# Kernel optimization log

Measured on AMD Instinct MI355X. Metric: run time of the kernel, lower is better.

The kernel has to match this reference:

```python
import jax, jax.numpy as jnp
import numpy as np


def setup_inputs() -> dict:
    key = jax.random.key(0)
    k1, k2, k3, k4 = jax.random.split(key, 4)
    B, S, D = 4, 2048, 1024
    return {
        "x": jax.random.normal(k1, (B, S, D), dtype=jnp.float32),
        "wq": jax.random.normal(k2, (D, D), dtype=jnp.float32),
        "wk": jax.random.normal(k3, (D, D), dtype=jnp.float32),
        "wv": jax.random.normal(k4, (D, D), dtype=jnp.float32),
    }


def reference(x, wq, wk, wv):
    # q,k,v: [B,S,D]
    q = x @ wq
    k = x @ wk
    v = x @ wv
    # NOTE: source applies NO 1/sqrt(d) scaling; we match it faithfully.
    scores = jnp.einsum("bsd,btd->bst", q, k)  # [B,S,S]
    weights = jax.nn.softmax(scores, axis=-1)
    return jnp.einsum("bst,btd->bsd", weights, v)  # [B,S,D]
```

## Files before the change

kernel.cpp:

```cpp
#include <hip/hip_runtime.h>


typedef _Float16 half4_t __attribute__((ext_vector_type(4)));
typedef _Float16 half8_t __attribute__((ext_vector_type(8)));
typedef float f32x4 __attribute__((ext_vector_type(4)));

#define BM 128
#define BN 128
#define BK 32

__device__ __forceinline__ void gl_lds16(const _Float16* g, _Float16* l) {
    __builtin_amdgcn_global_load_lds(
        (const __attribute__((address_space(1))) unsigned int*)g,
        (__attribute__((address_space(3))) unsigned int*)l, 16, 0, 0);
}

__global__ __launch_bounds__(256) void conv_all_kernel(
    const float* __restrict__ x, const float* __restrict__ wq,
    const float* __restrict__ wk, const float* __restrict__ wv,
    _Float16* __restrict__ xh, _Float16* __restrict__ xl,
    _Float16* __restrict__ qh, _Float16* __restrict__ ql,
    _Float16* __restrict__ kh, _Float16* __restrict__ kl,
    _Float16* __restrict__ vTh)
{
    __shared__ float tle[64][65];
    const int bid = blockIdx.x;
    if (bid < 10240) {
        const float* in;
        _Float16 *hi, *lo;
        int i0;
        if (bid < 8192)      { in = x;  hi = xh; lo = xl; i0 = bid; }
        else if (bid < 9216) { in = wq; hi = qh; lo = ql; i0 = bid - 8192; }
        else                 { in = wk; hi = kh; lo = kl; i0 = bid - 9216; }
        int i = i0 * 256 + threadIdx.x;
        float4 v = ((const float4*)in)[i];
        float xs[4] = {v.x, v.y, v.z, v.w};
        half4_t h, l;
#pragma unroll
        for (int j = 0; j < 4; ++j) {
            _Float16 hh = (_Float16)xs[j];
            h[j] = hh;
            l[j] = (_Float16)(xs[j] - (float)hh);
        }
        ((half4_t*)hi)[i] = h;
        ((half4_t*)lo)[i] = l;
    } else {
        const int t = bid - 10240;
        const int tr = (t >> 4) * 64, tc = (t & 15) * 64;
        const int t16 = threadIdx.x & 15, tq = threadIdx.x >> 4;
#pragma unroll
        for (int j = 0; j < 4; ++j) {
            int lr = tq + j * 16;
            float4 v = *(const float4*)(wv + (size_t)(tr + lr) * 1024 + tc + t16 * 4);
            tle[lr][t16 * 4 + 0] = v.x;
            tle[lr][t16 * 4 + 1] = v.y;
            tle[lr][t16 * 4 + 2] = v.z;
            tle[lr][t16 * 4 + 3] = v.w;
        }
        __syncthreads();
#pragma unroll
        for (int j = 0; j < 4; ++j) {
            int orow = tq + j * 16;
            int oc = t16 * 4;
            half4_t h;
#pragma unroll
            for (int i = 0; i < 4; ++i) h[i] = (_Float16)tle[oc + i][orow];
            *(half4_t*)(vTh + (size_t)(tc + orow) * 1024 + tr + oc) = h;
        }
    }
}

template <bool OUTF32>
__global__ __launch_bounds__(256) void gemm_split(
    const _Float16* __restrict__ Ah, const _Float16* __restrict__ Al, size_t az,
    const _Float16* __restrict__ Bh, const _Float16* __restrict__ Bl, size_t bz,
    float* __restrict__ Cf, size_t cz, int ldc,
    _Float16* __restrict__ Oh, _Float16* __restrict__ Ol, size_t oz, int ldo,
    int lda, int ldb, int K)
{
    __shared__ __align__(16) _Float16 sAh[BM][BK], sAl[BM][BK];
    __shared__ __align__(16) _Float16 sBh[BN][BK], sBl[BN][BK];

    const int tid = threadIdx.x;
    const int wave = tid >> 6, lane = tid & 63;
    const int wm = (wave >> 1) * 64, wn = (wave & 1) * 64;
    const int lrow = lane & 15, quad = lane >> 4;
    const int bm = blockIdx.y * BM, bn = blockIdx.x * BN;
    const int z = blockIdx.z;

    const _Float16* pAh = Ah + (size_t)z * az;
    const _Float16* pAl = Al + (size_t)z * az;
    const _Float16* pBh = Bh + (size_t)z * bz;
    const _Float16* pBl = Bl + (size_t)z * bz;

    const int r0 = wave * 32 + (lane >> 2);
    const int kofs = (lane & 3) * 8;
    const size_t a0o = (size_t)(bm + r0) * lda + kofs;
    const size_t a1o = a0o + (size_t)16 * lda;
    const size_t b0o = (size_t)(bn + r0) * ldb + kofs;
    const size_t b1o = b0o + (size_t)16 * ldb;
    _Float16* lA0 = &sAh[r0][kofs];
    _Float16* lA1 = &sAh[r0 + 16][kofs];
    _Float16* lAl0 = &sAl[r0][kofs];
    _Float16* lAl1 = &sAl[r0 + 16][kofs];
    _Float16* lB0 = &sBh[r0][kofs];
    _Float16* lB1 = &sBh[r0 + 16][kofs];
    _Float16* lBl0 = &sBl[r0][kofs];
    _Float16* lBl1 = &sBl[r0 + 16][kofs];

    f32x4 acc[4][4];
#pragma unroll
    for (int i = 0; i < 4; ++i)
#pragma unroll
        for (int j = 0; j < 4; ++j) acc[i][j] = 0.0f;

    for (int k0 = 0; k0 < K; k0 += BK) {
        gl_lds16(pAh + a0o + k0, lA0);
        gl_lds16(pAh + a1o + k0, lA1);
        gl_lds16(pAl + a0o + k0, lAl0);
        gl_lds16(pAl + a1o + k0, lAl1);
        gl_lds16(pBh + b0o + k0, lB0);
        gl_lds16(pBh + b1o + k0, lB1);
        gl_lds16(pBl + b0o + k0, lBl0);
        gl_lds16(pBl + b1o + k0, lBl1);
        __syncthreads();

        half8_t a0[4], a1[4], b0[4], b1[4];
#pragma unroll
        for (int mt = 0; mt < 4; ++mt) {
            a0[mt] = *(const half8_t*)&sAh[wm + mt * 16 + lrow][quad * 8];
            a1[mt] = *(const half8_t*)&sAl[wm + mt * 16 + lrow][quad * 8];
        }
#pragma unroll
        for (int nt = 0; nt < 4; ++nt) {
            b0[nt] = *(const half8_t*)&sBh[wn + nt * 16 + lrow][quad * 8];
            b1[nt] = *(const half8_t*)&sBl[wn + nt * 16 + lrow][quad * 8];
        }
#pragma unroll
        for (int mt = 0; mt < 4; ++mt)
#pragma unroll
            for (int nt = 0; nt < 4; ++nt) {
                acc[mt][nt] = __builtin_amdgcn_mfma_f32_16x16x32_f16(a0[mt], b0[nt], acc[mt][nt], 0, 0, 0);
                acc[mt][nt] = __builtin_amdgcn_mfma_f32_16x16x32_f16(a0[mt], b1[nt], acc[mt][nt], 0, 0, 0);
                acc[mt][nt] = __builtin_amdgcn_mfma_f32_16x16x32_f16(a1[mt], b0[nt], acc[mt][nt], 0, 0, 0);
            }
        __syncthreads();
    }

#pragma unroll
    for (int mt = 0; mt < 4; ++mt)
#pragma unroll
        for (int nt = 0; nt < 4; ++nt)
#pragma unroll
            for (int r = 0; r < 4; ++r) {
                int gm = bm + wm + mt * 16 + quad * 4 + r;
                int gn = bn + wn + nt * 16 + lrow;
                float v = acc[mt][nt][r];
                if (OUTF32) {
                    Cf[(size_t)z * cz + (size_t)gm * ldc + gn] = v;
                } else {
                    _Float16 h = (_Float16)v;
                    Oh[(size_t)z * oz + (size_t)gm * ldo + gn] = h;
                    Ol[(size_t)z * oz + (size_t)gm * ldo + gn] = (_Float16)(v - (float)h);
                }
            }
}

__global__ __launch_bounds__(256) void yv_kernel(
    const _Float16* __restrict__ xh, const _Float16* __restrict__ xl,
    const _Float16* __restrict__ Mh, const _Float16* __restrict__ Ml,
    const _Float16* __restrict__ wvTh,
    _Float16* __restrict__ yh, _Float16* __restrict__ yl,
    _Float16* __restrict__ vT)
{
    __shared__ __align__(16) char buf[128 * 132 * 2];

    const int tid = threadIdx.x;
    const int wave = tid >> 6, lane = tid & 63;
    const int wm = (wave >> 1) * 64, wn = (wave & 1) * 64;
    const int lrow = lane & 15, quad = lane >> 4;
    const int bm = blockIdx.y * BM, bn = blockIdx.x * BN;
    const bool vrole = (blockIdx.z != 0);

    const int r0 = wave * 32 + (lane >> 2);
    const int kofs = (lane & 3) * 8;
    const size_t a0o = (size_t)(bm + r0) * 1024 + kofs;
    const size_t a1o = a0o + (size_t)16 * 1024;
    const size_t b0o = (size_t)(bn + r0) * 1024 + kofs;
    const size_t b1o = b0o + (size_t)16 * 1024;

    f32x4 acc[4][4];
#pragma unroll
    for (int i = 0; i < 4; ++i)
#pragma unroll
        for (int j = 0; j < 4; ++j) acc[i][j] = 0.0f;

    _Float16* tle = (_Float16*)buf;

    if (!vrole) {
        _Float16* sAh = (_Float16*)buf;
        _Float16* sAl = (_Float16*)(buf + 8192);
        _Float16* sBh = (_Float16*)(buf + 16384);
        _Float16* sBl = (_Float16*)(buf + 24576);
        _Float16* lA0 = sAh + r0 * BK + kofs;
        _Float16* lA1 = sAh + (r0 + 16) * BK + kofs;
        _Float16* lAl0 = sAl + r0 * BK + kofs;
        _Float16* lAl1 = sAl + (r0 + 16) * BK + kofs;
        _Float16* lB0 = sBh + r0 * BK + kofs;
        _Float16* lB1 = sBh + (r0 + 16) * BK + kofs;
        _Float16* lBl0 = sBl + r0 * BK + kofs;
        _Float16* lBl1 = sBl + (r0 + 16) * BK + kofs;

        for (int k0 = 0; k0 < 1024; k0 += BK) {
            gl_lds16(xh + a0o + k0, lA0);
            gl_lds16(xh + a1o + k0, lA1);
            gl_lds16(xl + a0o + k0, lAl0);
            gl_lds16(xl + a1o + k0, lAl1);
            gl_lds16(Mh + b0o + k0, lB0);
            gl_lds16(Mh + b1o + k0, lB1);
            gl_lds16(Ml + b0o + k0, lBl0);
            gl_lds16(Ml + b1o + k0, lBl1);
            __syncthreads();

            half8_t a0[4], a1[4], b0[4], b1[4];
#pragma unroll
            for (int mt = 0; mt < 4; ++mt) {
                a0[mt] = *(const half8_t*)(sAh + (wm + mt * 16 + lrow) * BK + quad * 8);
                a1[mt] = *(const half8_t*)(sAl + (wm + mt * 16 + lrow) * BK + quad * 8);
            }
#pragma unroll
            for (int nt = 0; nt < 4; ++nt) {
                b0[nt] = *(const half8_t*)(sBh + (wn + nt * 16 + lrow) * BK + quad * 8);
                b1[nt] = *(const half8_t*)(sBl + (wn + nt * 16 + lrow) * BK + quad * 8);
            }
#pragma unroll
            for (int mt = 0; mt < 4; ++mt)
#pragma unroll
                for (int nt = 0; nt < 4; ++nt) {
                    acc[mt][nt] = __builtin_amdgcn_mfma_f32_16x16x32_f16(a0[mt], b0[nt], acc[mt][nt], 0, 0, 0);
                    acc[mt][nt] = __builtin_amdgcn_mfma_f32_16x16x32_f16(a0[mt], b1[nt], acc[mt][nt], 0, 0, 0);
                    acc[mt][nt] = __builtin_amdgcn_mfma_f32_16x16x32_f16(a1[mt], b0[nt], acc[mt][nt], 0, 0, 0);
                }
            __syncthreads();
        }

#pragma unroll
        for (int pass = 0; pass < 2; ++pass) {
            if (pass) __syncthreads();
#pragma unroll
            for (int mt = 0; mt < 4; ++mt)
#pragma unroll
                for (int nt = 0; nt < 4; ++nt) {
                    int rloc = wm + mt * 16 + quad * 4;
                    int cloc = wn + nt * 16 + lrow;
#pragma unroll
                    for (int r = 0; r < 4; ++r) {
                        float v = acc[mt][nt][r];
                        _Float16 h = (_Float16)v;
                        tle[(rloc + r) * 132 + cloc] =
                            pass == 0 ? h : (_Float16)(v - (float)h);
                    }
                }
            __syncthreads();
            _Float16* dst = pass == 0 ? yh : yl;
#pragma unroll
            for (int i = 0; i < 8; ++i) {
                int flat = i * 256 + tid;
                int rloc = flat >> 4, c = (flat & 15) * 8;
                half8_t o8;
#pragma unroll
                for (int j = 0; j < 8; ++j) o8[j] = tle[rloc * 132 + c + j];
                *(half8_t*)(dst + (size_t)(bm + rloc) * 1024 + bn + c) = o8;
            }
        }
    } else {
        _Float16* sA = (_Float16*)buf;
        _Float16* sB = (_Float16*)(buf + 8192);
        _Float16* lA0 = sA + r0 * BK + kofs;
        _Float16* lA1 = sA + (r0 + 16) * BK + kofs;
        _Float16* lB0 = sB + r0 * BK + kofs;
        _Float16* lB1 = sB + (r0 + 16) * BK + kofs;

        for (int k0 = 0; k0 < 1024; k0 += BK) {
            gl_lds16(xh + a0o + k0, lA0);
            gl_lds16(xh + a1o + k0, lA1);
            gl_lds16(wvTh + b0o + k0, lB0);
            gl_lds16(wvTh + b1o + k0, lB1);
            __syncthreads();

            half8_t a0[4], b0[4];
#pragma unroll
            for (int mt = 0; mt < 4; ++mt)
                a0[mt] = *(const half8_t*)(sA + (wm + mt * 16 + lrow) * BK + quad * 8);
#pragma unroll
            for (int nt = 0; nt < 4; ++nt)
                b0[nt] = *(const half8_t*)(sB + (wn + nt * 16 + lrow) * BK + quad * 8);
#pragma unroll
            for (int mt = 0; mt < 4; ++mt)
#pragma unroll
                for (int nt = 0; nt < 4; ++nt)
                    acc[mt][nt] = __builtin_amdgcn_mfma_f32_16x16x32_f16(a0[mt], b0[nt], acc[mt][nt], 0, 0, 0);
            __syncthreads();
        }

#pragma unroll
        for (int mt = 0; mt < 4; ++mt)
#pragma unroll
            for (int nt = 0; nt < 4; ++nt) {
                int t0 = wm + mt * 16 + quad * 4;
                int e_l = wn + nt * 16 + lrow;
                half4_t o;
#pragma unroll
                for (int r = 0; r < 4; ++r) o[r] = (_Float16)acc[mt][nt][r];
                *(half4_t*)(tle + e_l * 132 + t0) = o;
            }
        __syncthreads();
        const int b = bm >> 11, tb = bm & 2047;
#pragma unroll
        for (int i = 0; i < 8; ++i) {
            int flat = i * 256 + tid;
            int e_l = flat >> 4, c = (flat & 15) * 8;
            half8_t o8;
#pragma unroll
            for (int j = 0; j < 8; ++j) o8[j] = tle[e_l * 132 + c + j];
            *(half8_t*)(vT + ((size_t)b << 21) + (size_t)(bn + e_l) * 2048 + tb + c) = o8;
        }
    }
}

__global__ __launch_bounds__(256) void gemm_plain(
    const _Float16* __restrict__ Ag, size_t az,
    const _Float16* __restrict__ Bg, size_t bz,
    float* __restrict__ Cf, size_t cz, int ldc,
    int lda, int ldb, int K)
{
    __shared__ __align__(16) _Float16 sA[BM][BK], sB[BN][BK];

    const int tid = threadIdx.x;
    const int wave = tid >> 6, lane = tid & 63;
    const int wm = (wave >> 1) * 64, wn = (wave & 1) * 64;
    const int lrow = lane & 15, quad = lane >> 4;
    const int bm = blockIdx.y * BM, bn = blockIdx.x * BN;
    const int z = blockIdx.z;

    const _Float16* pA = Ag + (size_t)z * az;
    const _Float16* pB = Bg + (size_t)z * bz;

    const int r0 = wave * 32 + (lane >> 2);
    const int kofs = (lane & 3) * 8;
    const size_t a0o = (size_t)(bm + r0) * lda + kofs;
    const size_t a1o = a0o + (size_t)16 * lda;
    const size_t b0o = (size_t)(bn + r0) * ldb + kofs;
    const size_t b1o = b0o + (size_t)16 * ldb;
    _Float16* lA0 = &sA[r0][kofs];
    _Float16* lA1 = &sA[r0 + 16][kofs];
    _Float16* lB0 = &sB[r0][kofs];
    _Float16* lB1 = &sB[r0 + 16][kofs];

    f32x4 acc[4][4];
#pragma unroll
    for (int i = 0; i < 4; ++i)
#pragma unroll
        for (int j = 0; j < 4; ++j) acc[i][j] = 0.0f;

    for (int k0 = 0; k0 < K; k0 += BK) {
        gl_lds16(pA + a0o + k0, lA0);
        gl_lds16(pA + a1o + k0, lA1);
        gl_lds16(pB + b0o + k0, lB0);
        gl_lds16(pB + b1o + k0, lB1);
        __syncthreads();

        half8_t a0[4], b0[4];
#pragma unroll
        for (int mt = 0; mt < 4; ++mt)
            a0[mt] = *(const half8_t*)&sA[wm + mt * 16 + lrow][quad * 8];
#pragma unroll
        for (int nt = 0; nt < 4; ++nt)
            b0[nt] = *(const half8_t*)&sB[wn + nt * 16 + lrow][quad * 8];
#pragma unroll
        for (int mt = 0; mt < 4; ++mt)
#pragma unroll
            for (int nt = 0; nt < 4; ++nt)
                acc[mt][nt] = __builtin_amdgcn_mfma_f32_16x16x32_f16(a0[mt], b0[nt], acc[mt][nt], 0, 0, 0);
        __syncthreads();
    }

#pragma unroll
    for (int mt = 0; mt < 4; ++mt)
#pragma unroll
        for (int nt = 0; nt < 4; ++nt) {
            int gm0 = bm + wm + mt * 16 + quad * 4;
            int gn = bn + wn + nt * 16 + lrow;
#pragma unroll
            for (int r = 0; r < 4; ++r)
                Cf[(size_t)z * cz + (size_t)(gm0 + r) * ldc + gn] = acc[mt][nt][r];
        }
}

__global__ __launch_bounds__(256) void softmax_kernel(float* __restrict__ S)
{
    float* row = S + (size_t)blockIdx.x * 2048;
    float4* r4 = (float4*)row;
    const int tid = threadIdx.x;
    const int wave = tid >> 6, lane = tid & 63;

    float4 a = r4[tid], b = r4[tid + 256];
    float m = fmaxf(fmaxf(fmaxf(a.x, a.y), fmaxf(a.z, a.w)),
                    fmaxf(fmaxf(b.x, b.y), fmaxf(b.z, b.w)));
#pragma unroll
    for (int o = 32; o; o >>= 1) m = fmaxf(m, __shfl_xor(m, o));
    __shared__ float redm[4];
    __shared__ float reds[4];
    if (lane == 0) redm[wave] = m;
    __syncthreads();
    m = fmaxf(fmaxf(redm[0], redm[1]), fmaxf(redm[2], redm[3]));

    a.x = __expf(a.x - m); a.y = __expf(a.y - m);
    a.z = __expf(a.z - m); a.w = __expf(a.w - m);
    b.x = __expf(b.x - m); b.y = __expf(b.y - m);
    b.z = __expf(b.z - m); b.w = __expf(b.w - m);

    float s = a.x + a.y + a.z + a.w + b.x + b.y + b.z + b.w;
#pragma unroll
    for (int o = 32; o; o >>= 1) s += __shfl_xor(s, o);
    if (lane == 0) reds[wave] = s;
    __syncthreads();
    s = reds[0] + reds[1] + reds[2] + reds[3];

    float inv = 1.0f / s;
    _Float16* o16 = (_Float16*)row;
    half4_t ha, hb;
    ha[0] = (_Float16)(a.x * inv); ha[1] = (_Float16)(a.y * inv);
    ha[2] = (_Float16)(a.z * inv); ha[3] = (_Float16)(a.w * inv);
    hb[0] = (_Float16)(b.x * inv); hb[1] = (_Float16)(b.y * inv);
    hb[2] = (_Float16)(b.z * inv); hb[3] = (_Float16)(b.w * inv);
    ((half4_t*)o16)[tid] = ha;
    ((half4_t*)o16)[tid + 256] = hb;
}

extern "C" void kernel_launch(void* const* d_in, const int* in_sizes, int n_in,
                              void* d_out, int out_size, void* d_ws, size_t ws_size,
                              hipStream_t stream)
{
    const float* x  = (const float*)d_in[0];
    const float* wq = (const float*)d_in[1];
    const float* wk = (const float*)d_in[2];
    const float* wv = (const float*)d_in[3];
    float* out = (float*)d_out;

    const int S = 2048, D = 1024;
    char* ws = (char*)d_ws;

    _Float16* xh   = (_Float16*)(ws);
    _Float16* xl   = (_Float16*)(ws + (16ull << 20));
    _Float16* yh   = (_Float16*)(ws + (32ull << 20));
    _Float16* yl   = (_Float16*)(ws + (48ull << 20));
    _Float16* vT   = (_Float16*)(ws + (64ull << 20));
    _Float16* wqh  = (_Float16*)(ws + (80ull << 20));
    _Float16* wql  = (_Float16*)(ws + (82ull << 20));
    _Float16* wkh  = (_Float16*)(ws + (84ull << 20));
    _Float16* wkl  = (_Float16*)(ws + (86ull << 20));
    _Float16* wvTh = (_Float16*)(ws + (88ull << 20));
    _Float16* Mh   = (_Float16*)(ws + (90ull << 20));
    _Float16* Ml   = (_Float16*)(ws + (92ull << 20));
    float*    sc   = (float*)(ws + (94ull << 20));

    conv_all_kernel<<<dim3(10496), dim3(256), 0, stream>>>(
        x, wq, wk, wv, xh, xl, wqh, wql, wkh, wkl, wvTh);

    gemm_split<false><<<dim3(D / BN, D / BM, 1), dim3(256), 0, stream>>>(
        wkh, wkl, 0, wqh, wql, 0, nullptr, 0, 0, Mh, Ml, 0, D, D, D, D);

    yv_kernel<<<dim3(D / BN, 8192 / BM, 2), dim3(256), 0, stream>>>(
        xh, xl, Mh, Ml, wvTh, yh, yl, vT);

    gemm_split<true><<<dim3(S / BN, S / BM, 4), dim3(256), 0, stream>>>(
        yh, yl, (size_t)S * D, xh, xl, (size_t)S * D, sc, (size_t)S * S, S,
        nullptr, nullptr, 0, 0, D, D, D);

    softmax_kernel<<<dim3(4 * S), dim3(256), 0, stream>>>(sc);

    gemm_plain<<<dim3(D / BN, S / BM, 4), dim3(256), 0, stream>>>(
        (const _Float16*)sc, (size_t)S * 4096, vT, (size_t)D * S,
        out, (size_t)S * D, D, 4096, S, S);
}
```

Baseline: 409.0 us.

## Add 256x256 eight-phase pipelined scores GEMM kernel with split-fp16 segments

Replaces the generic split-precision scores GEMM with a dedicated kernel. It uses 512 threads, 256x256 tiles, and a multi-buffered LDS pipeline with direct global-to-LDS loads and an XOR swizzle. The K loop is split into 48 tiles that cover the hi*hi, lo*hi and hi*lo products, and loads for later tiles are interleaved with MFMA phases using barriers and priority hints. The goal is better data reuse and overlap of memory with compute. The cost is 64KB of LDS per block and fewer blocks in flight (8x8x4 = 256 blocks).

```diff
diff --git a/kernel.cpp b/kernel.cpp
--- a/kernel.cpp
+++ b/kernel.cpp
@@ -166,6 +166,144 @@
             }
 }
 
+#define NTILES 48
+
+__global__ __launch_bounds__(512, 2) void scores_8ph(
+    const _Float16* __restrict__ yh, const _Float16* __restrict__ yl,
+    const _Float16* __restrict__ xh, const _Float16* __restrict__ xl,
+    float* __restrict__ Cf)
+{
+    __shared__ __align__(16) _Float16 sA[4][8192];
+    __shared__ __align__(16) _Float16 sB[4][8192];
+
+    const int tid = threadIdx.x;
+    const int wave = tid >> 6, lane = tid & 63;
+    const int wm = (wave >> 2) * 128;
+    const int wn = (wave & 3) * 64;
+    const int l15 = lane & 15, jq = lane >> 4;
+    const int z = blockIdx.z;
+    const int bm = blockIdx.y * 256, bn = blockIdx.x * 256;
+
+    const _Float16* Ah = yh + ((size_t)z * 2048 + bm) * 1024;
+    const _Float16* Al = yl + ((size_t)z * 2048 + bm) * 1024;
+    const _Float16* Bh = xh + ((size_t)z * 2048 + bn) * 1024;
+    const _Float16* Bl = xl + ((size_t)z * 2048 + bn) * 1024;
+
+    auto stage = [&](const _Float16* base, int tloc, int khalf, _Float16* slot) {
+#pragma unroll
+        for (int i = 0; i < 2; ++i) {
+            int c = i * 512 + tid;
+            int row = c >> 2;
+            int j = (c & 3) ^ ((row >> 1) & 3);
+            gl_lds16(base + (size_t)row * 1024 + tloc * 64 + khalf * 32 + j * 8,
+                     slot + c * 8);
+        }
+    };
+    auto aseg = [&](int t) { return t < 32 ? Ah : Al; };
+    auto bseg = [&](int t) { return (t >> 4) == 1 ? Bl : Bh; };
+    auto frag = [&](const _Float16* slot, int row) {
+        int F = row * 4 + (jq ^ ((row >> 1) & 3));
+        return *(const half8_t*)(slot + F * 8);
+    };
+
+    f32x4 acc[8][4];
+#pragma unroll
+    for (int i = 0; i < 8; ++i)
+#pragma unroll
+        for (int j = 0; j < 4; ++j) acc[i][j] = 0.0f;
+
+    stage(aseg(0), 0, 0, sA[0]);
+    stage(bseg(0), 0, 0, sB[0]);
+    stage(aseg(0), 0, 1, sA[1]);
+    stage(bseg(0), 0, 1, sB[1]);
+    stage(aseg(1), 1, 0, sA[2]);
+    stage(bseg(1), 1, 0, sB[2]);
+    asm volatile("s_waitcnt vmcnt(4)\n\ts_barrier" ::: "memory");
+
+    for (int t = 0; t < NTILES; ++t) {
+        const int t1 = (t + 1 < NTILES) ? t + 1 : NTILES - 1;
+        const int t2 = (t + 2 < NTILES) ? t + 2 : NTILES - 1;
+        _Float16* a0s = sA[(t & 1) * 2 + 0];
+        _Float16* b0s = sB[(t & 1) * 2 + 0];
+        _Float16* a1s = sA[(t & 1) * 2 + 1];
+        _Float16* b1s = sB[(t & 1) * 2 + 1];
+        half8_t aa[4], bb[4];
+
+#pragma unroll
+        for (int n = 0; n < 4; ++n) bb[n] = frag(b0s, wn + n * 16 + l15);
+#pragma unroll
+        for (int m = 0; m < 4; ++m) aa[m] = frag(a0s, wm + m * 16 + l15);
+        stage(aseg(t1), t1 & 15, 1, sA[(t1 & 1) * 2 + 1]);
+        asm volatile("s_barrier" ::: "memory");
+        __builtin_amdgcn_s_setprio(1);
+#pragma unroll
+        for (int m = 0; m < 4; ++m)
+#pragma unroll
+            for (int n = 0; n < 4; ++n)
+                acc[m][n] = __builtin_amdgcn_mfma_f32_16x16x32_f16(aa[m], bb[n], acc[m][n], 0, 0, 0);
+        __builtin_amdgcn_s_setprio(0);
+        __builtin_amdgcn_sched_barrier(0);
+        asm volatile("s_barrier" ::: "memory");
+
+#pragma unroll
+        for (int m = 0; m < 4; ++m) aa[m] = frag(a0s, wm + 64 + m * 16 + l15);
+        stage(bseg(t1), t1 & 15, 1, sB[(t1 & 1) * 2 + 1]);
+        asm volatile("s_barrier" ::: "memory");
+        __builtin_amdgcn_s_setprio(1);
+#pragma unroll
+        for (int m = 0; m < 4; ++m)
+#pragma unroll
+            for (int n = 0; n < 4; ++n)
+                acc[4 + m][n] = __builtin_amdgcn_mfma_f32_16x16x32_f16(aa[m], bb[n], acc[4 + m][n], 0, 0, 0);
+        __builtin_amdgcn_s_setprio(0);
+        __builtin_amdgcn_sched_barrier(0);
+        asm volatile("s_barrier" ::: "memory");
+
+#pragma unroll
+        for (int n = 0; n < 4; ++n) bb[n] = frag(b1s, wn + n * 16 + l15);
+#pragma unroll
+        for (int m = 0; m < 4; ++m) aa[m] = frag(a1s, wm + m * 16 + l15);
+        stage(aseg(t2), t2 & 15, 0, sA[(t2 & 1) * 2 + 0]);
+        asm volatile("s_barrier" ::: "memory");
+        __builtin_amdgcn_s_setprio(1);
+#pragma unroll
+        for (int m = 0; m < 4; ++m)
+#pragma unroll
+            for (int n = 0; n < 4; ++n)
+                acc[m][n] = __builtin_amdgcn_mfma_f32_16x16x32_f16(aa[m], bb[n], acc[m][n], 0, 0, 0);
+        __builtin_amdgcn_s_setprio(0);
+        __builtin_amdgcn_sched_barrier(0);
+        asm volatile("s_barrier" ::: "memory");
+
+#pragma unroll
+        for (int m = 0; m < 4; ++m) aa[m] = frag(a1s, wm + 64 + m * 16 + l15);
+        stage(bseg(t2), t2 & 15, 0, sB[(t2 & 1) * 2 + 0]);
+        asm volatile("s_barrier" ::: "memory");
+        __builtin_amdgcn_s_setprio(1);
+#pragma unroll
+        for (int m = 0; m < 4; ++m)
+#pragma unroll
+            for (int n = 0; n < 4; ++n)
+                acc[4 + m][n] = __builtin_amdgcn_mfma_f32_16x16x32_f16(aa[m], bb[n], acc[4 + m][n], 0, 0, 0);
+        __builtin_amdgcn_s_setprio(0);
+        __builtin_amdgcn_sched_barrier(0);
+        asm volatile("s_waitcnt vmcnt(4)\n\ts_barrier" ::: "memory");
+    }
+    asm volatile("s_waitcnt vmcnt(0)" ::: "memory");
+
+    float* C = Cf + (size_t)z * 2048 * 2048;
+#pragma unroll
+    for (int mi = 0; mi < 8; ++mi)
+#pragma unroll
+        for (int ni = 0; ni < 4; ++ni) {
+            int gm0 = bm + wm + mi * 16 + jq * 4;
+            int gn = bn + wn + ni * 16 + l15;
+#pragma unroll
+            for (int r = 0; r < 4; ++r)
+                C[(size_t)(gm0 + r) * 2048 + gn] = acc[mi][ni][r];
+        }
+}
+
 __global__ __launch_bounds__(256) void yv_kernel(
     const _Float16* __restrict__ xh, const _Float16* __restrict__ xl,
     const _Float16* __restrict__ Mh, const _Float16* __restrict__ Ml,
@@ -474,9 +612,8 @@
     yv_kernel<<<dim3(D / BN, 8192 / BM, 2), dim3(256), 0, stream>>>(
         xh, xl, Mh, Ml, wvTh, yh, yl, vT);
 
-    gemm_split<true><<<dim3(S / BN, S / BM, 4), dim3(256), 0, stream>>>(
-        yh, yl, (size_t)S * D, xh, xl, (size_t)S * D, sc, (size_t)S * S, S,
-        nullptr, nullptr, 0, 0, D, D, D);
+    scores_8ph<<<dim3(S / 256, S / 256, 4), dim3(512), 0, stream>>>(
+        yh, yl, xh, xl, sc);
 
     softmax_kernel<<<dim3(4 * S), dim3(256), 0, stream>>>(sc);
 
```

Result: no change. 409.7 us (+0.2%).

## Replace split-precision scores GEMM with 256x256 eight-phase pipelined kernel

Applied to the files above, without the earlier changes.

Swaps the generic split-fp16 score GEMM for a dedicated kernel. It uses 256x256 tiles, 512 threads, a 4-slot LDS ring filled through direct global-to-LDS loads, and an eight-phase schedule that interleaves staging with MFMA, with priority raised around the math. Both tensors carry hi/lo halves, and only three products are computed (hi*hi, lo*hi, hi*lo) as 48 k-panels. Blocks are remapped to spread work across XCDs. The goal is more reuse per tile and hiding memory latency behind MFMA, at the cost of heavy register and LDS use and fragile barrier/waitcnt ordering.

```diff
diff --git a/kernel.cpp b/kernel.cpp
--- a/kernel.cpp
+++ b/kernel.cpp
@@ -166,6 +166,157 @@
             }
 }
 
+#define NTILES 48
+
+__global__ __launch_bounds__(512, 2) void scores_8ph(
+    const _Float16* __restrict__ yh, const _Float16* __restrict__ yl,
+    const _Float16* __restrict__ xh, const _Float16* __restrict__ xl,
+    float* __restrict__ Cf)
+{
+    __shared__ __align__(16) _Float16 sA[4][8192];
+    __shared__ __align__(16) _Float16 sB[4][8192];
+
+    const int tid = threadIdx.x;
+    const int wave = tid >> 6, lane = tid & 63;
+    const int wm = (wave >> 2) * 128;
+    const int wn = (wave & 3) * 64;
+    const int l15 = lane & 15, jq = lane >> 4;
+
+    const int flat = blockIdx.x + (blockIdx.y << 3) + (blockIdx.z << 6);
+    const int work = ((flat & 7) << 5) + (flat >> 3);
+    const int z = work >> 6;
+    const int bm = ((work >> 3) & 7) * 256;
+    const int bn = (work & 7) * 256;
+
+    const _Float16* Ah = yh + ((size_t)z * 2048 + bm) * 1024;
+    const _Float16* Al = yl + ((size_t)z * 2048 + bm) * 1024;
+    const _Float16* Bh = xh + ((size_t)z * 2048 + bn) * 1024;
+    const _Float16* Bl = xl + ((size_t)z * 2048 + bn) * 1024;
+
+    int a_off[8], b_off[4];
+#pragma unroll
+    for (int h = 0; h < 2; ++h)
+#pragma unroll
+        for (int m = 0; m < 4; ++m) {
+            int row = wm + h * 64 + m * 16 + l15;
+            int F = row * 4 + (jq ^ ((row >> 1) & 3));
+            a_off[h * 4 + m] = F * 16;
+            asm volatile("" : "+v"(a_off[h * 4 + m]));
+        }
+#pragma unroll
+    for (int n = 0; n < 4; ++n) {
+        int row = wn + n * 16 + l15;
+        int F = row * 4 + (jq ^ ((row >> 1) & 3));
+        b_off[n] = F * 16;
+        asm volatile("" : "+v"(b_off[n]));
+    }
+    int row0 = tid >> 2;
+    int j0 = (tid & 3) ^ ((row0 >> 1) & 3);
+    int g0 = row0 * 2048 + j0 * 16;
+    int g1 = g0 + 262144;
+    asm volatile("" : "+v"(g0), "+v"(g1));
+
+    _Float16* SA0 = sA[0]; _Float16* SA1 = sA[1];
+    _Float16* SA2 = sA[2]; _Float16* SA3 = sA[3];
+    _Float16* SB0 = sB[0]; _Float16* SB1 = sB[1];
+    _Float16* SB2 = sB[2]; _Float16* SB3 = sB[3];
+
+    auto STG = [&](const _Float16* p, _Float16* slot) {
+        gl_lds16((const _Float16*)((const char*)p + g0), slot + tid * 8);
+        gl_lds16((const _Float16*)((const char*)p + g1), slot + 4096 + tid * 8);
+    };
+    auto APAN = [&](int tt, int kh) {
+        return (tt < 32 ? Ah : Al) + (tt & 15) * 64 + kh * 32;
+    };
+    auto BPAN = [&](int tt, int kh) {
+        return ((tt >> 4) == 1 ? Bl : Bh) + (tt & 15) * 64 + kh * 32;
+    };
+    auto RDA = [&](const _Float16* slot, int half, half8_t* dst) {
+#pragma unroll
+        for (int m = 0; m < 4; ++m)
+            dst[m] = *(const half8_t*)((const char*)slot + a_off[half * 4 + m]);
+    };
+    auto RDB = [&](const _Float16* slot, half8_t* dst) {
+#pragma unroll
+        for (int n = 0; n < 4; ++n)
+            dst[n] = *(const half8_t*)((const char*)slot + b_off[n]);
+    };
+
+    f32x4 acc[8][4];
+#pragma unroll
+    for (int i = 0; i < 8; ++i)
+#pragma unroll
+        for (int j = 0; j < 4; ++j) acc[i][j] = 0.0f;
+
+    auto MM = [&](half8_t* aa, half8_t* bb, int ah) {
+#pragma unroll
+        for (int m = 0; m < 4; ++m)
+#pragma unroll
+            for (int n = 0; n < 4; ++n)
+                acc[ah * 4 + m][n] = __builtin_amdgcn_mfma_f32_16x16x32_f16(
+                    aa[m], bb[n], acc[ah * 4 + m][n], 0, 0, 0);
+    };
+
+#define BAR   asm volatile("s_barrier" ::: "memory")
+#define VMBAR asm volatile("s_waitcnt vmcnt(4)\n\ts_barrier" ::: "memory")
+#define P1    __builtin_amdgcn_s_setprio(1)
+#define P0    __builtin_amdgcn_s_setprio(0)
+
+    STG(APAN(0, 0), SA0); STG(BPAN(0, 0), SB0);
+    STG(APAN(0, 1), SA1); STG(BPAN(0, 1), SB1);
+    STG(APAN(1, 0), SA2); STG(BPAN(1, 0), SB2);
+    VMBAR;
+
+    for (int t = 0; t < NTILES; t += 2) {
+        const int u1 = t + 1;
+        const int u2 = (t + 2 < NTILES) ? t + 2 : NTILES - 1;
+        const int u3 = (t + 3 < NTILES) ? t + 3 : NTILES - 1;
+        half8_t aa[4], bb[4];
+
+        RDB(SB0, bb); RDA(SA0, 0, aa); STG(APAN(u1, 1), SA3);
+        BAR; P1; MM(aa, bb, 0); P0; BAR;
+
+        RDA(SA0, 1, aa); STG(BPAN(u1, 1), SB3);
+        BAR; P1; MM(aa, bb, 1); P0; BAR;
+
+        RDB(SB1, bb); RDA(SA1, 0, aa); STG(APAN(u2, 0), SA0);
+        BAR; P1; MM(aa, bb, 0); P0; BAR;
+
+        RDA(SA1, 1, aa); STG(BPAN(u2, 0), SB0);
+        BAR; P1; MM(aa, bb, 1); P0; VMBAR;
+
+        RDB(SB2, bb); RDA(SA2, 0, aa); STG(APAN(u2, 1), SA1);
+        BAR; P1; MM(aa, bb, 0); P0; BAR;
+
+        RDA(SA2, 1, aa); STG(BPAN(u2, 1), SB1);
+        BAR; P1; MM(aa, bb, 1); P0; BAR;
+
+        RDB(SB3, bb); RDA(SA3, 0, aa); STG(APAN(u3, 0), SA2);
+        BAR; P1; MM(aa, bb, 0); P0; BAR;
+
+        RDA(SA3, 1, aa); STG(BPAN(u3, 0), SB2);
+        BAR; P1; MM(aa, bb, 1); P0; VMBAR;
+    }
+    asm volatile("s_waitcnt vmcnt(0)" ::: "memory");
+
+#undef BAR
+#undef VMBAR
+#undef P1
+#undef P0
+
+    float* C = Cf + (size_t)z * 2048 * 2048;
+#pragma unroll
+    for (int mi = 0; mi < 8; ++mi)
+#pragma unroll
+        for (int ni = 0; ni < 4; ++ni) {
+            int gm0 = bm + wm + mi * 16 + jq * 4;
+            int gn = bn + wn + ni * 16 + l15;
+#pragma unroll
+            for (int r = 0; r < 4; ++r)
+                C[(size_t)(gm0 + r) * 2048 + gn] = acc[mi][ni][r];
+        }
+}
+
 __global__ __launch_bounds__(256) void yv_kernel(
     const _Float16* __restrict__ xh, const _Float16* __restrict__ xl,
     const _Float16* __restrict__ Mh, const _Float16* __restrict__ Ml,
@@ -474,9 +625,8 @@
     yv_kernel<<<dim3(D / BN, 8192 / BM, 2), dim3(256), 0, stream>>>(
         xh, xl, Mh, Ml, wvTh, yh, yl, vT);
 
-    gemm_split<true><<<dim3(S / BN, S / BM, 4), dim3(256), 0, stream>>>(
-        yh, yl, (size_t)S * D, xh, xl, (size_t)S * D, sc, (size_t)S * S, S,
-        nullptr, nullptr, 0, 0, D, D, D);
+    scores_8ph<<<dim3(S / 256, S / 256, 4), dim3(512), 0, stream>>>(
+        yh, yl, xh, xl, sc);
 
     softmax_kernel<<<dim3(4 * S), dim3(256), 0, stream>>>(sc);
 
```

New measurement: 409.3 us. Within noise of the previous version (+0.1%).

## Replace split-precision scores GEMM with 256x256-tile 16-wave double-buffered kernel

Applied to the files above, without the earlier changes.

Swaps the 128x128-tile gemm_split for the scores GEMM with a new 1024-thread kernel computing 256x256 tiles. It uses register-staged, XOR-swizzled double-buffered LDS panels and 16x16x32 f16 MFMAs, and runs the hi/lo split terms as 96 K-steps over three panel pairs. It also remaps blocks for L2 locality and raises wave priority around the MFMAs. The aim is more data reuse per tile and better overlap of global loads with compute, at the cost of higher register and LDS use and lower occupancy.

```diff
diff --git a/kernel.cpp b/kernel.cpp
--- a/kernel.cpp
+++ b/kernel.cpp
@@ -166,6 +166,111 @@
             }
 }
 
+#define NSTEPS 96
+
+__global__ __launch_bounds__(1024) void scores_16w(
+    const _Float16* __restrict__ yh, const _Float16* __restrict__ yl,
+    const _Float16* __restrict__ xh, const _Float16* __restrict__ xl,
+    float* __restrict__ Cf)
+{
+    __shared__ __align__(16) _Float16 sA[2][8192];
+    __shared__ __align__(16) _Float16 sB[2][8192];
+
+    const int tid = threadIdx.x;
+    const int wave = tid >> 6, lane = tid & 63;
+    const int wm = (wave >> 2) * 64;
+    const int wn = (wave & 3) * 64;
+    const int l15 = lane & 15, jq = lane >> 4;
+
+    const int flat = blockIdx.x + (blockIdx.y << 3) + (blockIdx.z << 6);
+    const int work = ((flat & 7) << 5) + (flat >> 3);
+    const int z = work >> 6;
+    const int bm = ((work >> 3) & 7) * 256;
+    const int bn = (work & 7) * 256;
+
+    const _Float16* Ah = yh + ((size_t)z * 2048 + bm) * 1024;
+    const _Float16* Al = yl + ((size_t)z * 2048 + bm) * 1024;
+    const _Float16* Bh = xh + ((size_t)z * 2048 + bn) * 1024;
+    const _Float16* Bl = xl + ((size_t)z * 2048 + bn) * 1024;
+
+    int a_off0, b_off0;
+    {
+        int row = wm + l15;
+        a_off0 = (row * 4 + (jq ^ ((row >> 1) & 3))) * 16;
+        row = wn + l15;
+        b_off0 = (row * 4 + (jq ^ ((row >> 1) & 3))) * 16;
+    }
+    int row0 = tid >> 2;
+    int j0 = (tid & 3) ^ ((row0 >> 1) & 3);
+    int g0 = row0 * 2048 + j0 * 16;
+    int wb0 = tid * 16;
+
+    f32x4 rA, rB;
+
+    auto ISSUE = [&](const _Float16* pa, const _Float16* pb) {
+        rA = *(const f32x4*)((const char*)pa + g0);
+        rB = *(const f32x4*)((const char*)pb + g0);
+    };
+    auto WRITE = [&](_Float16* slotA, _Float16* slotB) {
+        *(f32x4*)((char*)slotA + wb0) = rA;
+        *(f32x4*)((char*)slotB + wb0) = rB;
+    };
+    auto APAN = [&](int t) { return (t < 64 ? Ah : Al) + (t & 31) * 32; };
+    auto BPAN = [&](int t) { return (((t >> 5) == 1) ? Bl : Bh) + (t & 31) * 32; };
+
+    f32x4 acc[4][4];
+#pragma unroll
+    for (int i = 0; i < 4; ++i)
+#pragma unroll
+        for (int j = 0; j < 4; ++j) acc[i][j] = 0.0f;
+
+    auto STEP = [&](const _Float16* sa, const _Float16* sb,
+                    _Float16* wa, _Float16* wb, int tn) {
+        half8_t fa[4], fb[4];
+#pragma unroll
+        for (int m = 0; m < 4; ++m)
+            fa[m] = *(const half8_t*)((const char*)sa + a_off0 + m * 1024);
+#pragma unroll
+        for (int n = 0; n < 4; ++n)
+            fb[n] = *(const half8_t*)((const char*)sb + b_off0 + n * 1024);
+        WRITE(wa, wb);
+        ISSUE(APAN(tn), BPAN(tn));
+        __builtin_amdgcn_s_setprio(1);
+#pragma unroll
+        for (int m = 0; m < 4; ++m)
+#pragma unroll
+            for (int n = 0; n < 4; ++n)
+                acc[m][n] = __builtin_amdgcn_mfma_f32_16x16x32_f16(
+                    fa[m], fb[n], acc[m][n], 0, 0, 0);
+        __builtin_amdgcn_s_setprio(0);
+        __builtin_amdgcn_s_barrier();
+    };
+
+    ISSUE(APAN(0), BPAN(0));
+    WRITE(sA[0], sB[0]);
+    ISSUE(APAN(1), BPAN(1));
+    __syncthreads();
+
+    for (int t = 0; t < NSTEPS; t += 2) {
+        const int t2 = (t + 2 < NSTEPS) ? t + 2 : NSTEPS - 1;
+        const int t3 = (t + 3 < NSTEPS) ? t + 3 : NSTEPS - 1;
+        STEP(sA[0], sB[0], sA[1], sB[1], t2);
+        STEP(sA[1], sB[1], sA[0], sB[0], t3);
+    }
+
+    float* C = Cf + (size_t)z * 2048 * 2048;
+#pragma unroll
+    for (int mi = 0; mi < 4; ++mi)
+#pragma unroll
+        for (int ni = 0; ni < 4; ++ni) {
+            int gm0 = bm + wm + mi * 16 + jq * 4;
+            int gn = bn + wn + ni * 16 + l15;
+#pragma unroll
+            for (int r = 0; r < 4; ++r)
+                C[(size_t)(gm0 + r) * 2048 + gn] = acc[mi][ni][r];
+        }
+}
+
 __global__ __launch_bounds__(256) void yv_kernel(
     const _Float16* __restrict__ xh, const _Float16* __restrict__ xl,
     const _Float16* __restrict__ Mh, const _Float16* __restrict__ Ml,
@@ -474,9 +579,8 @@
     yv_kernel<<<dim3(D / BN, 8192 / BM, 2), dim3(256), 0, stream>>>(
         xh, xl, Mh, Ml, wvTh, yh, yl, vT);
 
-    gemm_split<true><<<dim3(S / BN, S / BM, 4), dim3(256), 0, stream>>>(
-        yh, yl, (size_t)S * D, xh, xl, (size_t)S * D, sc, (size_t)S * S, S,
-        nullptr, nullptr, 0, 0, D, D, D);
+    scores_16w<<<dim3(S / 256, S / 256, 4), dim3(1024), 0, stream>>>(
+        yh, yl, xh, xl, sc);
 
     softmax_kernel<<<dim3(4 * S), dim3(256), 0, stream>>>(sc);
 
```

Result: no change. 406.2 us (-0.7%).
